# Kernel optimization log

Hardware: AMD Instinct MI355X
Metric: run time of the kernel (lower is better)

## Reference

```python
import jax, jax.numpy as jnp
import numpy as np

X_SIZE = 256
H_SIZE = 512
N_CHILDREN = 32768


def setup_inputs() -> dict:
    key = jax.random.key(0)
    ks = jax.random.split(key, 7)
    x = jax.random.normal(ks[0], (X_SIZE,), dtype=jnp.float32)
    hs = jax.random.normal(ks[1], (N_CHILDREN, H_SIZE), dtype=jnp.float32)
    cs = jax.random.normal(ks[2], (N_CHILDREN, H_SIZE), dtype=jnp.float32)
    # xavier-uniform-ish init for weights, zeros for biases
    def xavier(k, shape):
        fan_in, fan_out = shape[-1], shape[-2]
        limit = float(np.sqrt(6.0 / (fan_in + fan_out)))
        return jax.random.uniform(k, shape, jnp.float32, -limit, limit)
    w_iou = xavier(ks[3], (3, H_SIZE, X_SIZE))
    u_iou = xavier(ks[4], (3, H_SIZE, H_SIZE))
    b_iou = jnp.zeros((3, H_SIZE), jnp.float32)
    w_f = xavier(ks[5], (H_SIZE, X_SIZE))
    u_f = xavier(ks[6], (H_SIZE, H_SIZE))
    b_f = jnp.zeros((H_SIZE, 1), jnp.float32)
    return {"x": x, "hs": hs, "cs": cs, "w_iou": w_iou, "u_iou": u_iou,
            "b_iou": b_iou, "w_f": w_f, "u_f": u_f, "b_f": b_f}


def reference(x, hs, cs, w_iou, u_iou, b_iou, w_f, u_f, b_f):
    # Child-sum Tree-LSTM cell for a single node.
    h_sum = hs.sum(axis=0)                                    # (h,)
    iou = (jnp.einsum('khx,x->kh', w_iou, x)
           + jnp.einsum('khg,g->kh', u_iou, h_sum)
           + b_iou)                                            # (3, h)
    i, o, u = iou[0], iou[1], iou[2]
    # fs: (h, n_children) forget gates, one per child
    fs = (w_f @ x)[:, None] + jnp.einsum('hg,ng->hn', u_f, hs) + b_f
    i = jax.nn.sigmoid(i)
    o = jax.nn.sigmoid(o)
    fs = jax.nn.sigmoid(fs)
    u = jnp.tanh(u)
    c = i * u + jnp.sum(fs * cs.T, axis=1)                    # (h,)
    h = o * jnp.tanh(c)
    return (h, c)
```

## Files before the change

### kernel.cpp

```cpp
#include <hip/hip_runtime.h>
#include <stdint.h>
#include <stddef.h>

#define H 512
#define XD 256
#define NCHLD 32768
#define NB 128
#define KT 32
#define NKT (H / KT)
#define NCT (NB / 16)

typedef float f32x4 __attribute__((ext_vector_type(4)));
typedef _Float16 f16x8 __attribute__((ext_vector_type(8)));
typedef _Float16 f16x4 __attribute__((ext_vector_type(4)));


__device__ __forceinline__ float sigm(float x) { return 1.0f / (1.0f + __expf(-x)); }

__device__ __forceinline__ f16x8 load_a_f16(const float* __restrict__ p) {
    float4 a = *(const float4*)p;
    float4 b = *(const float4*)(p + 4);
    f16x8 r;
    r[0] = (_Float16)a.x; r[1] = (_Float16)a.y; r[2] = (_Float16)a.z; r[3] = (_Float16)a.w;
    r[4] = (_Float16)b.x; r[5] = (_Float16)b.y; r[6] = (_Float16)b.z; r[7] = (_Float16)b.w;
    return r;
}

__global__ __launch_bounds__(256) void k0_setup(const float* __restrict__ x,
                                                const float* __restrict__ w_f,
                                                const float* __restrict__ b_f,
                                                float* __restrict__ ws) {
    const int gid = blockIdx.x * 256 + threadIdx.x;
    const int row = gid >> 2;
    const int part = gid & 3;
    const float4* wr = (const float4*)(w_f + (size_t)row * XD) + part * 16;
    const float4* xv = (const float4*)x + part * 16;
    float acc = 0.0f;
#pragma unroll 4
    for (int i = 0; i < 16; ++i) {
        float4 a = wr[i], b = xv[i];
        acc += a.x * b.x + a.y * b.y + a.z * b.z + a.w * b.w;
    }
    acc += __shfl_xor(acc, 1);
    acc += __shfl_xor(acc, 2);
    if (part == 0) {
        ws[row]        = acc + b_f[row];
        ws[512 + row]  = 0.0f;
        ws[1024 + row] = 0.0f;
    }
}

__global__ __launch_bounds__(1024) void k2_main(const float* __restrict__ hs,
                                                const float* __restrict__ cs,
                                                const float* __restrict__ u_f,
                                                float* __restrict__ ws) {
    __shared__ _Float16 hs_s[2][NB][KT];
    __shared__ float hsum_l[H];

    const float* pre_f  = ws;
    float* c_acc   = ws + 512;
    float* h_sum_g = ws + 1024;

    const int tid  = threadIdx.x;
    const int wid  = tid >> 6;
    const int lane = tid & 63;
    const int c0   = blockIdx.x * NB;

    if (tid < H) hsum_l[tid] = 0.0f;

    const int sc  = tid >> 3;
    const int skg = tid & 7;
    const float* hs_src = hs + (size_t)(c0 + sc) * H + skg * 4;

    f32x4 acc[2][NCT];
    const f32x4 vzero = {0.0f, 0.0f, 0.0f, 0.0f};
#pragma unroll
    for (int rt = 0; rt < 2; ++rt)
#pragma unroll
        for (int ct = 0; ct < NCT; ++ct)
            acc[rt][ct] = vzero;

    const int arow  = wid * 32 + (lane & 15);
    const int akgrp = (lane >> 4) * 8;
    const float* a0p = u_f + (size_t)arow * H + akgrp;
    const float* a1p = u_f + (size_t)(arow + 16) * H + akgrp;

    const int bcol = lane & 15;
    const int bk   = (lane >> 4) * 8;

    float4 ld0 = *(const float4*)(hs_src);
    __syncthreads();
    {
        float4 v = ld0;
#pragma unroll
        for (int m = 8; m <= 32; m <<= 1) {
            v.x += __shfl_xor(v.x, m);
            v.y += __shfl_xor(v.y, m);
            v.z += __shfl_xor(v.z, m);
            v.w += __shfl_xor(v.w, m);
        }
        if ((lane >> 3) == 0) {
            const int d = skg * 4;
            atomicAdd(&hsum_l[d + 0], v.x);
            atomicAdd(&hsum_l[d + 1], v.y);
            atomicAdd(&hsum_l[d + 2], v.z);
            atomicAdd(&hsum_l[d + 3], v.w);
        }
        f16x4 st;
        st[0] = (_Float16)ld0.x; st[1] = (_Float16)ld0.y;
        st[2] = (_Float16)ld0.z; st[3] = (_Float16)ld0.w;
        *(f16x4*)&hs_s[0][sc][skg * 4] = st;
    }
    __syncthreads();

    for (int kk = 0; kk < NKT; ++kk) {
        const int cur = kk & 1;
        const bool more = (kk + 1 < NKT);
        float4 nld;
        if (more) nld = *(const float4*)(hs_src + (size_t)(kk + 1) * KT);

        f16x8 af0 = load_a_f16(a0p + (size_t)kk * KT);
        f16x8 af1 = load_a_f16(a1p + (size_t)kk * KT);
#pragma unroll
        for (int ct = 0; ct < NCT; ++ct) {
            f16x8 bf = *(const f16x8*)&hs_s[cur][ct * 16 + bcol][bk];
            acc[0][ct] = __builtin_amdgcn_mfma_f32_16x16x32_f16(af0, bf, acc[0][ct], 0, 0, 0);
            acc[1][ct] = __builtin_amdgcn_mfma_f32_16x16x32_f16(af1, bf, acc[1][ct], 0, 0, 0);
        }
        __syncthreads();
        if (more) {
            float4 v = nld;
#pragma unroll
            for (int m = 8; m <= 32; m <<= 1) {
                v.x += __shfl_xor(v.x, m);
                v.y += __shfl_xor(v.y, m);
                v.z += __shfl_xor(v.z, m);
                v.w += __shfl_xor(v.w, m);
            }
            if ((lane >> 3) == 0) {
                const int d = (kk + 1) * KT + skg * 4;
                atomicAdd(&hsum_l[d + 0], v.x);
                atomicAdd(&hsum_l[d + 1], v.y);
                atomicAdd(&hsum_l[d + 2], v.z);
                atomicAdd(&hsum_l[d + 3], v.w);
            }
            f16x4 st;
            st[0] = (_Float16)nld.x; st[1] = (_Float16)nld.y;
            st[2] = (_Float16)nld.z; st[3] = (_Float16)nld.w;
            *(f16x4*)&hs_s[cur ^ 1][sc][skg * 4] = st;
            __syncthreads();
        }
    }

    if (tid < H) atomicAdd(&h_sum_g[tid], hsum_l[tid]);

    const int g4 = (lane >> 4) * 4;
#pragma unroll
    for (int rt = 0; rt < 2; ++rt) {
        const int rbase = wid * 32 + rt * 16 + g4;
        float4 pf = *(const float4*)(pre_f + rbase);
        f32x4 csum = vzero;
#pragma unroll
        for (int ct = 0; ct < NCT; ++ct) {
            const int child = c0 + ct * 16 + (lane & 15);
            float4 cv = *(const float4*)(cs + (size_t)child * H + rbase);
            csum[0] += sigm(acc[rt][ct][0] + pf.x) * cv.x;
            csum[1] += sigm(acc[rt][ct][1] + pf.y) * cv.y;
            csum[2] += sigm(acc[rt][ct][2] + pf.z) * cv.z;
            csum[3] += sigm(acc[rt][ct][3] + pf.w) * cv.w;
        }
#pragma unroll
        for (int m = 1; m <= 8; m <<= 1) {
            csum[0] += __shfl_xor(csum[0], m);
            csum[1] += __shfl_xor(csum[1], m);
            csum[2] += __shfl_xor(csum[2], m);
            csum[3] += __shfl_xor(csum[3], m);
        }
        if ((lane & 15) == 0) {
            atomicAdd(&c_acc[rbase + 0], csum[0]);
            atomicAdd(&c_acc[rbase + 1], csum[1]);
            atomicAdd(&c_acc[rbase + 2], csum[2]);
            atomicAdd(&c_acc[rbase + 3], csum[3]);
        }
    }
}

__global__ __launch_bounds__(256) void k3_iou(const float* __restrict__ x,
                                              const float* __restrict__ w_iou,
                                              const float* __restrict__ u_iou,
                                              const float* __restrict__ b_iou,
                                              float* __restrict__ ws) {
    const int gid = blockIdx.x * 256 + threadIdx.x;
    const int row = gid >> 2;
    const int part = gid & 3;
    const float* hsum = ws + 1024;
    float acc = 0.0f;
    const float4* wr = (const float4*)(w_iou + (size_t)row * XD) + part * 16;
    const float4* xv = (const float4*)x + part * 16;
#pragma unroll 4
    for (int i = 0; i < 16; ++i) {
        float4 a = wr[i], b = xv[i];
        acc += a.x * b.x + a.y * b.y + a.z * b.z + a.w * b.w;
    }
    const float4* ur = (const float4*)(u_iou + (size_t)row * H) + part * 32;
    const float4* hv = (const float4*)hsum + part * 32;
#pragma unroll 4
    for (int i = 0; i < 32; ++i) {
        float4 a = ur[i], b = hv[i];
        acc += a.x * b.x + a.y * b.y + a.z * b.z + a.w * b.w;
    }
    acc += __shfl_xor(acc, 1);
    acc += __shfl_xor(acc, 2);
    if (part == 0) ws[1536 + row] = acc + b_iou[row];
}

__global__ __launch_bounds__(512) void k4_fin(const float* __restrict__ ws,
                                              float* __restrict__ out) {
    const int h = threadIdx.x;
    const float iv = ws[1536 + h];
    const float ov = ws[1536 + 512 + h];
    const float uv = ws[1536 + 1024 + h];
    const float i = sigm(iv);
    const float o = sigm(ov);
    const float u = tanhf(uv);
    const float c = i * u + ws[512 + h];
    out[h]       = o * tanhf(c);
    out[512 + h] = c;
}

extern "C" void kernel_launch(void* const* d_in, const int* in_sizes, int n_in,
                              void* d_out, int out_size, void* d_ws, size_t ws_size,
                              hipStream_t stream) {
    const float* x     = (const float*)d_in[0];
    const float* hs    = (const float*)d_in[1];
    const float* cs    = (const float*)d_in[2];
    const float* w_iou = (const float*)d_in[3];
    const float* u_iou = (const float*)d_in[4];
    const float* b_iou = (const float*)d_in[5];
    const float* w_f   = (const float*)d_in[6];
    const float* u_f   = (const float*)d_in[7];
    const float* b_f   = (const float*)d_in[8];
    float* ws  = (float*)d_ws;
    float* out = (float*)d_out;

    k0_setup<<<8, 256, 0, stream>>>(x, w_f, b_f, ws);
    k2_main<<<NCHLD / NB, 1024, 0, stream>>>(hs, cs, u_f, ws);
    k3_iou<<<24, 256, 0, stream>>>(x, w_iou, u_iou, b_iou, ws);
    k4_fin<<<1, 512, 0, stream>>>(ws, out);
}
```

Before: 251.1 us.

## Pre-convert u_f to fp16, retile main GEMM, shard atomics, widen iou kernel

u_f is converted to fp16 once in the setup kernel, so the main kernel loads fp16 A fragments directly instead of converting fp32 each tile. Each main block now covers 64 children with 512 threads, and each wave handles 64 rows with 4 row tiles, which raises A-fragment reuse per B load. The LDS tile is padded to reduce bank conflicts, and hs prefetch runs two stages ahead with one barrier per step. Global atomics for c_acc and h_sum are spread over 4 shards that later kernels sum back together, and the iou kernel uses 8 threads per row. The setup kernel gains a conversion pass and twice as many main blocks stream u_f.

```diff
diff --git a/kernel.cpp b/kernel.cpp
--- a/kernel.cpp
+++ b/kernel.cpp
@@ -5,159 +5,167 @@
 #define H 512
 #define XD 256
 #define NCHLD 32768
-#define NB 128
+#define NB 64
 #define KT 32
-#define NKT (H / KT)
-#define NCT (NB / 16)
+#define NKT 16
+#define NCT 4
+#define NRT 4
+#define LDSP 40
+#define NSHARD 4
+
+#define WS_PREF 0
+#define WS_CACC 512
+#define WS_HSUM 2560
+#define WS_IOU  4608
+#define WS_UF16 8192
 
 typedef float f32x4 __attribute__((ext_vector_type(4)));
 typedef _Float16 f16x8 __attribute__((ext_vector_type(8)));
 typedef _Float16 f16x4 __attribute__((ext_vector_type(4)));
 
-
 __device__ __forceinline__ float sigm(float x) { return 1.0f / (1.0f + __expf(-x)); }
-
-__device__ __forceinline__ f16x8 load_a_f16(const float* __restrict__ p) {
-    float4 a = *(const float4*)p;
-    float4 b = *(const float4*)(p + 4);
-    f16x8 r;
-    r[0] = (_Float16)a.x; r[1] = (_Float16)a.y; r[2] = (_Float16)a.z; r[3] = (_Float16)a.w;
-    r[4] = (_Float16)b.x; r[5] = (_Float16)b.y; r[6] = (_Float16)b.z; r[7] = (_Float16)b.w;
-    return r;
-}
 
 __global__ __launch_bounds__(256) void k0_setup(const float* __restrict__ x,
                                                 const float* __restrict__ w_f,
                                                 const float* __restrict__ b_f,
-                                                float* __restrict__ ws) {
-    const int gid = blockIdx.x * 256 + threadIdx.x;
-    const int row = gid >> 2;
-    const int part = gid & 3;
-    const float4* wr = (const float4*)(w_f + (size_t)row * XD) + part * 16;
-    const float4* xv = (const float4*)x + part * 16;
-    float acc = 0.0f;
-#pragma unroll 4
-    for (int i = 0; i < 16; ++i) {
-        float4 a = wr[i], b = xv[i];
-        acc += a.x * b.x + a.y * b.y + a.z * b.z + a.w * b.w;
-    }
-    acc += __shfl_xor(acc, 1);
-    acc += __shfl_xor(acc, 2);
-    if (part == 0) {
-        ws[row]        = acc + b_f[row];
-        ws[512 + row]  = 0.0f;
-        ws[1024 + row] = 0.0f;
-    }
-}
-
-__global__ __launch_bounds__(1024) void k2_main(const float* __restrict__ hs,
-                                                const float* __restrict__ cs,
                                                 const float* __restrict__ u_f,
                                                 float* __restrict__ ws) {
-    __shared__ _Float16 hs_s[2][NB][KT];
+    const int b = blockIdx.x;
+    if (b < 256) {
+        const int i = (b * 256 + threadIdx.x) * 4;
+        float4 v = *(const float4*)(u_f + i);
+        f16x4 h;
+        h[0] = (_Float16)v.x; h[1] = (_Float16)v.y;
+        h[2] = (_Float16)v.z; h[3] = (_Float16)v.w;
+        *(f16x4*)((_Float16*)(ws + WS_UF16) + i) = h;
+    } else {
+        const int gid = (b - 256) * 256 + threadIdx.x;
+        const int row = gid >> 2;
+        const int part = gid & 3;
+        const float4* wr = (const float4*)(w_f + (size_t)row * XD) + part * 16;
+        const float4* xv = (const float4*)x + part * 16;
+        float acc = 0.0f;
+#pragma unroll 4
+        for (int i = 0; i < 16; ++i) {
+            float4 a = wr[i], c = xv[i];
+            acc += a.x * c.x + a.y * c.y + a.z * c.z + a.w * c.w;
+        }
+        acc += __shfl_xor(acc, 1);
+        acc += __shfl_xor(acc, 2);
+        if (part == 0) ws[WS_PREF + row] = acc + b_f[row];
+        ws[WS_CACC + gid] = 0.0f;
+        ws[WS_HSUM + gid] = 0.0f;
+    }
+}
+
+__global__ __launch_bounds__(512, 4) void k2_main(const float* __restrict__ hs,
+                                                  const float* __restrict__ cs,
+                                                  float* __restrict__ ws) {
+    __shared__ _Float16 bt[2][NB][LDSP];
     __shared__ float hsum_l[H];
 
-    const float* pre_f  = ws;
-    float* c_acc   = ws + 512;
-    float* h_sum_g = ws + 1024;
+    const _Float16* uf16 = (const _Float16*)(ws + WS_UF16);
+    const float* pre_f = ws + WS_PREF;
+    float* c_acc = ws + WS_CACC + (blockIdx.x & (NSHARD - 1)) * H;
+    float* h_sum = ws + WS_HSUM + (blockIdx.x & (NSHARD - 1)) * H;
 
     const int tid  = threadIdx.x;
     const int wid  = tid >> 6;
     const int lane = tid & 63;
     const int c0   = blockIdx.x * NB;
 
-    if (tid < H) hsum_l[tid] = 0.0f;
-
     const int sc  = tid >> 3;
     const int skg = tid & 7;
-    const float* hs_src = hs + (size_t)(c0 + sc) * H + skg * 4;
-
-    f32x4 acc[2][NCT];
+    const float* hsrc = hs + (size_t)(c0 + sc) * H + skg * 4;
+    _Float16* stp0 = &bt[0][sc][skg * 4];
+    _Float16* stp1 = &bt[1][sc][skg * 4];
+
+    const int arow = wid * 64 + (lane & 15);
+    const int ak   = (lane >> 4) * 8;
+    const _Float16* abase = uf16 + (size_t)arow * H + ak;
+
+    const int bcol = lane & 15;
+    const int bk   = (lane >> 4) * 8;
+
+    f32x4 acc[NRT][NCT];
     const f32x4 vzero = {0.0f, 0.0f, 0.0f, 0.0f};
 #pragma unroll
-    for (int rt = 0; rt < 2; ++rt)
+    for (int rt = 0; rt < NRT; ++rt)
 #pragma unroll
         for (int ct = 0; ct < NCT; ++ct)
             acc[rt][ct] = vzero;
 
-    const int arow  = wid * 32 + (lane & 15);
-    const int akgrp = (lane >> 4) * 8;
-    const float* a0p = u_f + (size_t)arow * H + akgrp;
-    const float* a1p = u_f + (size_t)(arow + 16) * H + akgrp;
-
-    const int bcol = lane & 15;
-    const int bk   = (lane >> 4) * 8;
-
-    float4 ld0 = *(const float4*)(hs_src);
+    if (tid < H) hsum_l[tid] = 0.0f;
+
+    float4 ra = *(const float4*)(hsrc);
+    float4 rb = *(const float4*)(hsrc + KT);
     __syncthreads();
+
     {
-        float4 v = ld0;
+        f16x4 h;
+        h[0] = (_Float16)ra.x; h[1] = (_Float16)ra.y;
+        h[2] = (_Float16)ra.z; h[3] = (_Float16)ra.w;
+        *(f16x4*)stp0 = h;
+        float4 v = ra;
 #pragma unroll
         for (int m = 8; m <= 32; m <<= 1) {
-            v.x += __shfl_xor(v.x, m);
-            v.y += __shfl_xor(v.y, m);
-            v.z += __shfl_xor(v.z, m);
-            v.w += __shfl_xor(v.w, m);
+            v.x += __shfl_xor(v.x, m); v.y += __shfl_xor(v.y, m);
+            v.z += __shfl_xor(v.z, m); v.w += __shfl_xor(v.w, m);
         }
         if ((lane >> 3) == 0) {
             const int d = skg * 4;
-            atomicAdd(&hsum_l[d + 0], v.x);
-            atomicAdd(&hsum_l[d + 1], v.y);
-            atomicAdd(&hsum_l[d + 2], v.z);
-            atomicAdd(&hsum_l[d + 3], v.w);
-        }
-        f16x4 st;
-        st[0] = (_Float16)ld0.x; st[1] = (_Float16)ld0.y;
-        st[2] = (_Float16)ld0.z; st[3] = (_Float16)ld0.w;
-        *(f16x4*)&hs_s[0][sc][skg * 4] = st;
+            atomicAdd(&hsum_l[d + 0], v.x); atomicAdd(&hsum_l[d + 1], v.y);
+            atomicAdd(&hsum_l[d + 2], v.z); atomicAdd(&hsum_l[d + 3], v.w);
+        }
     }
     __syncthreads();
 
+#pragma unroll
     for (int kk = 0; kk < NKT; ++kk) {
-        const int cur = kk & 1;
-        const bool more = (kk + 1 < NKT);
-        float4 nld;
-        if (more) nld = *(const float4*)(hs_src + (size_t)(kk + 1) * KT);
-
-        f16x8 af0 = load_a_f16(a0p + (size_t)kk * KT);
-        f16x8 af1 = load_a_f16(a1p + (size_t)kk * KT);
+        if (kk + 2 < NKT) ra = *(const float4*)(hsrc + (size_t)(kk + 2) * KT);
+
+        f16x8 af[NRT];
+#pragma unroll
+        for (int rt = 0; rt < NRT; ++rt)
+            af[rt] = *(const f16x8*)(abase + (size_t)rt * 16 * H + kk * KT);
+
+        const _Float16* bbase = &bt[kk & 1][0][0];
 #pragma unroll
         for (int ct = 0; ct < NCT; ++ct) {
-            f16x8 bf = *(const f16x8*)&hs_s[cur][ct * 16 + bcol][bk];
-            acc[0][ct] = __builtin_amdgcn_mfma_f32_16x16x32_f16(af0, bf, acc[0][ct], 0, 0, 0);
-            acc[1][ct] = __builtin_amdgcn_mfma_f32_16x16x32_f16(af1, bf, acc[1][ct], 0, 0, 0);
-        }
-        __syncthreads();
-        if (more) {
-            float4 v = nld;
+            f16x8 bf = *(const f16x8*)(bbase + (ct * 16 + bcol) * LDSP + bk);
+#pragma unroll
+            for (int rt = 0; rt < NRT; ++rt)
+                acc[rt][ct] = __builtin_amdgcn_mfma_f32_16x16x32_f16(af[rt], bf, acc[rt][ct], 0, 0, 0);
+        }
+
+        if (kk + 1 < NKT) {
+            _Float16* stp = (kk & 1) ? stp0 : stp1;
+            f16x4 h;
+            h[0] = (_Float16)rb.x; h[1] = (_Float16)rb.y;
+            h[2] = (_Float16)rb.z; h[3] = (_Float16)rb.w;
+            *(f16x4*)stp = h;
+            float4 v = rb;
 #pragma unroll
             for (int m = 8; m <= 32; m <<= 1) {
-                v.x += __shfl_xor(v.x, m);
-                v.y += __shfl_xor(v.y, m);
-                v.z += __shfl_xor(v.z, m);
-                v.w += __shfl_xor(v.w, m);
+                v.x += __shfl_xor(v.x, m); v.y += __shfl_xor(v.y, m);
+                v.z += __shfl_xor(v.z, m); v.w += __shfl_xor(v.w, m);
             }
             if ((lane >> 3) == 0) {
                 const int d = (kk + 1) * KT + skg * 4;
-                atomicAdd(&hsum_l[d + 0], v.x);
-                atomicAdd(&hsum_l[d + 1], v.y);
-                atomicAdd(&hsum_l[d + 2], v.z);
-                atomicAdd(&hsum_l[d + 3], v.w);
+                atomicAdd(&hsum_l[d + 0], v.x); atomicAdd(&hsum_l[d + 1], v.y);
+                atomicAdd(&hsum_l[d + 2], v.z); atomicAdd(&hsum_l[d + 3], v.w);
             }
-            f16x4 st;
-            st[0] = (_Float16)nld.x; st[1] = (_Float16)nld.y;
-            st[2] = (_Float16)nld.z; st[3] = (_Float16)nld.w;
-            *(f16x4*)&hs_s[cur ^ 1][sc][skg * 4] = st;
-            __syncthreads();
-        }
-    }
-
-    if (tid < H) atomicAdd(&h_sum_g[tid], hsum_l[tid]);
+        }
+        __syncthreads();
+        rb = ra;
+    }
+
+    if (tid < H) atomicAdd(&h_sum[tid], hsum_l[tid]);
 
     const int g4 = (lane >> 4) * 4;
 #pragma unroll
-    for (int rt = 0; rt < 2; ++rt) {
-        const int rbase = wid * 32 + rt * 16 + g4;
+    for (int rt = 0; rt < NRT; ++rt) {
+        const int rbase = wid * 64 + rt * 16 + g4;
         float4 pf = *(const float4*)(pre_f + rbase);
         f32x4 csum = vzero;
 #pragma unroll
@@ -171,16 +179,12 @@
         }
 #pragma unroll
         for (int m = 1; m <= 8; m <<= 1) {
-            csum[0] += __shfl_xor(csum[0], m);
-            csum[1] += __shfl_xor(csum[1], m);
-            csum[2] += __shfl_xor(csum[2], m);
-            csum[3] += __shfl_xor(csum[3], m);
+            csum[0] += __shfl_xor(csum[0], m); csum[1] += __shfl_xor(csum[1], m);
+            csum[2] += __shfl_xor(csum[2], m); csum[3] += __shfl_xor(csum[3], m);
         }
         if ((lane & 15) == 0) {
-            atomicAdd(&c_acc[rbase + 0], csum[0]);
-            atomicAdd(&c_acc[rbase + 1], csum[1]);
-            atomicAdd(&c_acc[rbase + 2], csum[2]);
-            atomicAdd(&c_acc[rbase + 3], csum[3]);
+            atomicAdd(&c_acc[rbase + 0], csum[0]); atomicAdd(&c_acc[rbase + 1], csum[1]);
+            atomicAdd(&c_acc[rbase + 2], csum[2]); atomicAdd(&c_acc[rbase + 3], csum[3]);
         }
     }
 }
@@ -191,39 +195,45 @@
                                               const float* __restrict__ b_iou,
                                               float* __restrict__ ws) {
     const int gid = blockIdx.x * 256 + threadIdx.x;
-    const int row = gid >> 2;
-    const int part = gid & 3;
-    const float* hsum = ws + 1024;
+    const int row = gid >> 3;
+    const int part = gid & 7;
     float acc = 0.0f;
-    const float4* wr = (const float4*)(w_iou + (size_t)row * XD) + part * 16;
-    const float4* xv = (const float4*)x + part * 16;
+    const float4* wr = (const float4*)(w_iou + (size_t)row * XD) + part * 8;
+    const float4* xv = (const float4*)x + part * 8;
+#pragma unroll
+    for (int i = 0; i < 8; ++i) {
+        float4 a = wr[i], b = xv[i];
+        acc += a.x * b.x + a.y * b.y + a.z * b.z + a.w * b.w;
+    }
+    const float4* ur = (const float4*)(u_iou + (size_t)row * H) + part * 16;
+    const float4* h0 = (const float4*)(ws + WS_HSUM) + part * 16;
+    const float4* h1 = h0 + 128;
+    const float4* h2 = h1 + 128;
+    const float4* h3 = h2 + 128;
 #pragma unroll 4
     for (int i = 0; i < 16; ++i) {
-        float4 a = wr[i], b = xv[i];
-        acc += a.x * b.x + a.y * b.y + a.z * b.z + a.w * b.w;
-    }
-    const float4* ur = (const float4*)(u_iou + (size_t)row * H) + part * 32;
-    const float4* hv = (const float4*)hsum + part * 32;
-#pragma unroll 4
-    for (int i = 0; i < 32; ++i) {
-        float4 a = ur[i], b = hv[i];
-        acc += a.x * b.x + a.y * b.y + a.z * b.z + a.w * b.w;
+        float4 a = ur[i];
+        float4 b0 = h0[i], b1 = h1[i], b2 = h2[i], b3 = h3[i];
+        acc += a.x * (b0.x + b1.x + b2.x + b3.x);
+        acc += a.y * (b0.y + b1.y + b2.y + b3.y);
+        acc += a.z * (b0.z + b1.z + b2.z + b3.z);
+        acc += a.w * (b0.w + b1.w + b2.w + b3.w);
     }
     acc += __shfl_xor(acc, 1);
     acc += __shfl_xor(acc, 2);
-    if (part == 0) ws[1536 + row] = acc + b_iou[row];
+    acc += __shfl_xor(acc, 4);
+    if (part == 0) ws[WS_IOU + row] = acc + b_iou[row];
 }
 
 __global__ __launch_bounds__(512) void k4_fin(const float* __restrict__ ws,
                                               float* __restrict__ out) {
     const int h = threadIdx.x;
-    const float iv = ws[1536 + h];
-    const float ov = ws[1536 + 512 + h];
-    const float uv = ws[1536 + 1024 + h];
-    const float i = sigm(iv);
-    const float o = sigm(ov);
-    const float u = tanhf(uv);
-    const float c = i * u + ws[512 + h];
+    const float i = sigm(ws[WS_IOU + h]);
+    const float o = sigm(ws[WS_IOU + 512 + h]);
+    const float u = tanhf(ws[WS_IOU + 1024 + h]);
+    const float cacc = ws[WS_CACC + h] + ws[WS_CACC + 512 + h] +
+                       ws[WS_CACC + 1024 + h] + ws[WS_CACC + 1536 + h];
+    const float c = i * u + cacc;
     out[h]       = o * tanhf(c);
     out[512 + h] = c;
 }
@@ -243,8 +253,8 @@
     float* ws  = (float*)d_ws;
     float* out = (float*)d_out;
 
-    k0_setup<<<8, 256, 0, stream>>>(x, w_f, b_f, ws);
-    k2_main<<<NCHLD / NB, 1024, 0, stream>>>(hs, cs, u_f, ws);
-    k3_iou<<<24, 256, 0, stream>>>(x, w_iou, u_iou, b_iou, ws);
+    k0_setup<<<264, 256, 0, stream>>>(x, w_f, b_f, u_f, ws);
+    k2_main<<<NCHLD / NB, 512, 0, stream>>>(hs, cs, ws);
+    k3_iou<<<48, 256, 0, stream>>>(x, w_iou, u_iou, b_iou, ws);
     k4_fin<<<1, 512, 0, stream>>>(ws, out);
 }
```

Result: faster. 213.6 us (-14.9%).
